# Performance work log

Measured on AMD Instinct MI355X. Metric: run time of the kernel, lower is better.

Reference implementation:

```python
import jax, jax.numpy as jnp
from jax import lax
import numpy as np

T, B, I, H = 512, 256, 13, 512


def setup_inputs() -> dict:
    key = jax.random.key(0)
    ks = jax.random.split(key, 8)
    s_ih = 1.0 / np.sqrt(H)
    # PyTorch LSTM params: gates stacked in order (i, f, g, o)
    x = jax.random.normal(ks[0], (T, B, I), dtype=jnp.float32)
    W_ih = jax.random.uniform(ks[1], (4 * H, I), minval=-s_ih, maxval=s_ih, dtype=jnp.float32)
    W_hh = jax.random.uniform(ks[2], (4 * H, H), minval=-s_ih, maxval=s_ih, dtype=jnp.float32)
    b_ih = jax.random.uniform(ks[3], (4 * H,), minval=-s_ih, maxval=s_ih, dtype=jnp.float32)
    b_hh = jax.random.uniform(ks[4], (4 * H,), minval=-s_ih, maxval=s_ih, dtype=jnp.float32)
    W_out = jax.random.uniform(ks[5], (1, H), minval=-s_ih, maxval=s_ih, dtype=jnp.float32)
    b_out = jax.random.uniform(ks[6], (1,), minval=-s_ih, maxval=s_ih, dtype=jnp.float32)
    return {"x": x, "W_ih": W_ih, "W_hh": W_hh, "b_ih": b_ih, "b_hh": b_hh,
            "W_out": W_out, "b_out": b_out}


def reference(x, W_ih, W_hh, b_ih, b_hh, W_out, b_out):
    # Precompute input-to-hidden gate projections for all timesteps (one big GEMM).
    # xg: [T, B, 4H]
    xg = jnp.einsum('tbi,gi->tbg', x, W_ih) + b_ih + b_hh
    h0 = jnp.zeros((x.shape[1], W_hh.shape[1]), dtype=x.dtype)

    def step(carry, xg_t):
        h, c = carry
        g = xg_t + h @ W_hh.T                      # [B, 4H]
        i, f, gg, o = jnp.split(g, 4, axis=-1)     # PyTorch gate order i,f,g,o
        i = jax.nn.sigmoid(i)
        f = jax.nn.sigmoid(f)
        gg = jnp.tanh(gg)
        o = jax.nn.sigmoid(o)
        c = f * c + i * gg
        h = o * jnp.tanh(c)
        return (h, c), h

    _, hs = lax.scan(step, (h0, h0), xg)           # hs: [T, B, H]
    y = jax.nn.relu(hs) @ W_out.T + b_out          # [T, B, 1]
    return y
```

## Files before the change

kernel.cpp:

```cpp
#include <hip/hip_runtime.h>
#include <hip/hip_bf16.h>

#define TT 512
#define BB 256
#define II 13
#define HH 512
#define NBLK 256
#define NTH 256
#define NKT 17
#define NSL 34
#define PS2 (NSL * 512)
#define GST 18
#define XROW (BB * II)

typedef __attribute__((ext_vector_type(8))) short short8;
typedef __attribute__((ext_vector_type(4))) float floatx4;
typedef __attribute__((ext_vector_type(4))) int intx4;

__device__ inline float sigm(float v) { return 1.f / (1.f + __expf(-v)); }
__device__ inline float tanh_(float v) {
    float e = __expf(-2.f * fabsf(v));
    float t = (1.f - e) / (1.f + e);
    return v < 0.f ? -t : t;
}
__device__ inline void split_bits(float v, unsigned short* hi, unsigned short* lo) {
    __hip_bfloat16 h = __float2bfloat16(v);
    float r = v - __bfloat162float(h);
    __hip_bfloat16 l = __float2bfloat16(r);
    *hi = __builtin_bit_cast(unsigned short, h);
    *lo = __builtin_bit_cast(unsigned short, l);
}
__device__ inline unsigned short bf16_bits(float v) {
    return __builtin_bit_cast(unsigned short, __float2bfloat16(v));
}

__device__ inline unsigned poll_mall(const unsigned* p) {
    unsigned v;
    asm volatile("global_load_dword %0, %1, off sc0 sc1\n\ts_waitcnt vmcnt(0)"
                 : "=&v"(v) : "v"(p) : "memory");
    return v;
}
__device__ inline void arrive_mall(unsigned* p) {
    asm volatile("global_atomic_add %0, %1, off sc1" :: "v"(p), "v"(1u) : "memory");
}
__device__ inline intx4 load_b128_l2(const void* p) {
    intx4 v;
    asm volatile("global_load_dwordx4 %0, %1, off sc0" : "=v"(v) : "v"(p));
    return v;
}
__device__ inline void store_short_l2(void* p, unsigned short v) {
    unsigned vv = v;
    asm volatile("global_store_short %0, %1, off sc0" :: "v"(p), "v"(vv) : "memory");
}
__device__ inline void store_dword_l2(void* p, unsigned v) {
    asm volatile("global_store_dword %0, %1, off sc0" :: "v"(p), "v"(v) : "memory");
}
__device__ inline void store_f32_wt(float* p, float v) {
    asm volatile("global_store_dword %0, %1, off sc0 sc1" :: "v"(p), "v"(v) : "memory");
}

__device__ inline void barrier_xcd(unsigned* cnt, unsigned target) {
    __syncthreads();
    if (threadIdx.x == 0) {
        arrive_mall(cnt);
        int guard = 0;
        unsigned v;
        do { v = poll_mall(cnt); } while ((int)(v - target) < 0 && ++guard < (1 << 16));
    }
    __syncthreads();
}

__global__ void __launch_bounds__(NTH, 1)
lstm_persist(const float* __restrict__ X,   const float* __restrict__ Wih,
             const float* __restrict__ Whh, const float* __restrict__ bih,
             const float* __restrict__ bhh, const float* __restrict__ Wout,
             const float* __restrict__ bout, float* __restrict__ Y,
             unsigned short* __restrict__ hbuf, unsigned* __restrict__ bars)
{
    extern __shared__ char smem[];
    unsigned short* Wf = (unsigned short*)smem;
    float* gbuf = (float*)(Wf + 4 * 2 * NKT * 512);
    int* shint = (int*)(gbuf + 128 * GST);

    const int tid = threadIdx.x;

    if (tid == 0) {
        unsigned x = __builtin_amdgcn_s_getreg(20 | (3 << 11)) & 7u;
        unsigned r = __hip_atomic_fetch_add(bars + 256 + x * 16, 1u,
                        __ATOMIC_RELAXED, __HIP_MEMORY_SCOPE_AGENT);
        shint[0] = (int)x;
        shint[1] = (int)(r & 31u);
    }
    __syncthreads();
    const int bc = shint[0];
    const int hs = shint[1];
    unsigned* bcnt = bars + bc * 32;

#define REGION(buf) (((buf) * 8 + bc) * PS2)

    {
        unsigned* hw = (unsigned*)hbuf;
        store_dword_l2(hw + (REGION(0) >> 1) + hs * 256 + tid, 0u);
        store_dword_l2(hw + (REGION(1) >> 1) + hs * 256 + tid, 0u);
        if (hs == 0) {
            for (int e = tid; e < 2 * 1024; e += NTH) {
                int buf = e >> 10, off = e & 1023;
                int row = (off >> 4) & 31, col = off & 15;
                unsigned short vh = 0;
                if (off < 512) {
                    if (col == 13) vh = 0x3F80u;
                    else if (col < 13 && buf == 0)
                        vh = bf16_bits(X[(bc * 32 + row) * II + col]);
                }
                store_short_l2(hbuf + REGION(buf) + 32 * 512 + off, vh);
            }
        }
        const float b0 = bout[0];
        for (int i = tid; i < 16 * 32; i += NTH) {
            int tr = hs * 16 + (i >> 5), cb = bc * 32 + (i & 31);
            store_f32_wt(&Y[tr * BB + cb], b0);
        }
    }
    for (int n = 0; n < 64; ++n) {
        int gate = n >> 4, hl = n & 15;
        int gr = gate * HH + hs * 16 + hl;
        for (int k = tid; k < 544; k += NTH) {
            float v;
            if (k < HH)            v = Whh[gr * HH + k];
            else if (k < HH + II)  v = Wih[gr * II + (k - HH)];
            else if (k == HH + II) v = bih[gr] + bhh[gr];
            else                   v = 0.f;
            unsigned short hi, lo; split_bits(v, &hi, &lo);
            const int slot = (hl + 16 * ((k & 31) >> 3)) * 8 + (k & 7);
            Wf[((gate * 2 + 0) * NKT + (k >> 5)) * 512 + slot] = hi;
            Wf[((gate * 2 + 1) * NKT + (k >> 5)) * 512 + slot] = lo;
        }
    }
    const int e0 = 2 * tid;
    const bool stv = (e0 < 32 * II);
    const int bl0 = e0 / II, xc0 = e0 - bl0 * II;
    const int e1 = e0 + 1;
    const int bl1 = e1 / II, xc1 = e1 - bl1 * II;
    float xr0 = 0.f, xr1 = 0.f;
    if (hs == 1 && stv) {
        const float2 v = *(const float2*)(X + XROW + bc * (32 * II) + e0);
        xr0 = v.x; xr1 = v.y;
    }

    barrier_xcd(bcnt, 32u);

    const int lane = tid & 63, wid = tid >> 6;
    const int mt = wid & 1;
    const int gp = wid >> 1;
    const int r15  = lane & 15;
    const int kgo  = (lane >> 4) * 8;
    const int slb  = kgo >> 4;
    const int lanehoff = (mt * 16 + r15) * 16 + (kgo & 8);
    const int lane8 = lane * 8;
    const unsigned short* F0 = Wf + ((4 * gp + 0) * NKT) * 512 + lane8;
    const unsigned short* F1 = Wf + ((4 * gp + 1) * NKT) * 512 + lane8;
    const unsigned short* F2 = Wf + ((4 * gp + 2) * NKT) * 512 + lane8;
    const unsigned short* F3 = Wf + ((4 * gp + 3) * NKT) * 512 + lane8;
    float c0 = 0.f, c1 = 0.f;
    const int ebl2 = tid >> 3;
    const int ej   = (tid & 7) * 2;
    const float2 wout2 = *(const float2*)&Wout[hs * 16 + ej];

    float ypend = 0.f;
    int   ycur  = bc * 32 + ebl2;

    for (int t = 0; t < TT; ++t) {
        const int cur = t & 1, nxt = cur ^ 1;
        const unsigned short* Ac = hbuf + REGION(cur) + lanehoff;

        intx4 ah[NKT];
#pragma unroll
        for (int kt = 0; kt < NKT; ++kt)
            ah[kt] = load_b128_l2(Ac + (kt * 2 + slb) * 512);
        __builtin_amdgcn_sched_barrier(0);
        if ((tid & 7) == 0)
            atomicAdd(&Y[ycur], ypend);
        __builtin_amdgcn_sched_barrier(0);

        short8 w0[4], w1[4], w2[4], w3[4];
#pragma unroll
        for (int j = 0; j < 4; ++j) {
            w0[j] = *(const short8*)(F0 + j * 512);
            w1[j] = *(const short8*)(F1 + j * 512);
            w2[j] = *(const short8*)(F2 + j * 512);
            w3[j] = *(const short8*)(F3 + j * 512);
        }
        floatx4 aA0 = {0,0,0,0}, aB0 = {0,0,0,0};
        floatx4 aA1 = {0,0,0,0}, aB1 = {0,0,0,0};

        asm volatile("s_waitcnt vmcnt(10)" ::: "memory");
        __builtin_amdgcn_sched_barrier(0);
#pragma unroll
        for (int kt = 0; kt < 8; ++kt) {
            short8 bh0 = w0[kt & 3], bv0 = w1[kt & 3];
            short8 bh1 = w2[kt & 3], bv1 = w3[kt & 3];
            if (kt + 4 < NKT) {
                w0[kt & 3] = *(const short8*)(F0 + (kt + 4) * 512);
                w1[kt & 3] = *(const short8*)(F1 + (kt + 4) * 512);
                w2[kt & 3] = *(const short8*)(F2 + (kt + 4) * 512);
                w3[kt & 3] = *(const short8*)(F3 + (kt + 4) * 512);
            }
            short8 chi = __builtin_bit_cast(short8, ah[kt]);
            aA0 = __builtin_amdgcn_mfma_f32_16x16x32_bf16(chi, bh0, aA0, 0, 0, 0);
            aA1 = __builtin_amdgcn_mfma_f32_16x16x32_bf16(chi, bh1, aA1, 0, 0, 0);
            aB0 = __builtin_amdgcn_mfma_f32_16x16x32_bf16(chi, bv0, aB0, 0, 0, 0);
            aB1 = __builtin_amdgcn_mfma_f32_16x16x32_bf16(chi, bv1, aB1, 0, 0, 0);
        }
        asm volatile("s_waitcnt vmcnt(1)" ::: "memory");
        __builtin_amdgcn_sched_barrier(0);
#pragma unroll
        for (int kt = 8; kt < NKT; ++kt) {
            short8 bh0 = w0[kt & 3], bv0 = w1[kt & 3];
            short8 bh1 = w2[kt & 3], bv1 = w3[kt & 3];
            if (kt + 4 < NKT) {
                w0[kt & 3] = *(const short8*)(F0 + (kt + 4) * 512);
                w1[kt & 3] = *(const short8*)(F1 + (kt + 4) * 512);
                w2[kt & 3] = *(const short8*)(F2 + (kt + 4) * 512);
                w3[kt & 3] = *(const short8*)(F3 + (kt + 4) * 512);
            }
            short8 chi = __builtin_bit_cast(short8, ah[kt]);
            aA0 = __builtin_amdgcn_mfma_f32_16x16x32_bf16(chi, bh0, aA0, 0, 0, 0);
            aA1 = __builtin_amdgcn_mfma_f32_16x16x32_bf16(chi, bh1, aA1, 0, 0, 0);
            aB0 = __builtin_amdgcn_mfma_f32_16x16x32_bf16(chi, bv0, aB0, 0, 0, 0);
            aB1 = __builtin_amdgcn_mfma_f32_16x16x32_bf16(chi, bv1, aB1, 0, 0, 0);
        }
        floatx4 acc0 = aA0 + aB0;
        floatx4 acc1 = aA1 + aB1;

        {
            const int b0r = mt * 16 + (lane >> 4) * 4;
            const int g0 = gp * 2;
#pragma unroll
            for (int r = 0; r < 4; ++r) {
                gbuf[((g0    ) * 32 + b0r + r) * GST + r15] = acc0[r];
                gbuf[((g0 + 1) * 32 + b0r + r) * GST + r15] = acc1[r];
            }
        }
        __syncthreads();
        {
            const float2 gi = *(const float2*)&gbuf[(0 * 32 + ebl2) * GST + ej];
            const float2 gf = *(const float2*)&gbuf[(1 * 32 + ebl2) * GST + ej];
            const float2 gg = *(const float2*)&gbuf[(2 * 32 + ebl2) * GST + ej];
            const float2 go = *(const float2*)&gbuf[(3 * 32 + ebl2) * GST + ej];

            c0 = sigm(gf.x) * c0 + sigm(gi.x) * tanh_(gg.x);
            float ha = sigm(go.x) * tanh_(c0);
            c1 = sigm(gf.y) * c1 + sigm(gi.y) * tanh_(gg.y);
            float hb = sigm(go.y) * tanh_(c1);

            unsigned* hw = (unsigned*)hbuf;
            store_dword_l2(hw + (REGION(nxt) >> 1) + hs * 256 + ebl2 * 8 + (tid & 7),
                           (unsigned)bf16_bits(ha) | ((unsigned)bf16_bits(hb) << 16));

            float p = fmaxf(ha, 0.f) * wout2.x + fmaxf(hb, 0.f) * wout2.y;
#pragma unroll
            for (int s = 4; s >= 1; s >>= 1)
                p += __shfl_xor(p, s);
            ypend = p;
            ycur  = t * BB + bc * 32 + ebl2;
        }
        if (t + 1 < TT && hs == ((t + 1) & 31) && stv) {
            store_short_l2(hbuf + REGION(nxt) + 32 * 512 + bl0 * 16 + xc0,
                           bf16_bits(xr0));
            store_short_l2(hbuf + REGION(nxt) + 32 * 512 + bl1 * 16 + xc1,
                           bf16_bits(xr1));
        }
        if (t + 2 < TT && hs == ((t + 2) & 31) && stv) {
            const float2 v = *(const float2*)(X + (t + 2) * XROW + bc * (32 * II) + e0);
            xr0 = v.x; xr1 = v.y;
        }
        if (t + 1 < TT)
            barrier_xcd(bcnt, 32u * (unsigned)(t + 2));
    }
    if ((tid & 7) == 0)
        atomicAdd(&Y[ycur], ypend);
}

extern "C" void kernel_launch(void* const* d_in, const int* in_sizes, int n_in,
                              void* d_out, int out_size, void* d_ws, size_t ws_size,
                              hipStream_t stream) {
    (void)in_sizes; (void)n_in; (void)out_size; (void)ws_size;
    const float* X    = (const float*)d_in[0];
    const float* Wih  = (const float*)d_in[1];
    const float* Whh  = (const float*)d_in[2];
    const float* bih  = (const float*)d_in[3];
    const float* bhh  = (const float*)d_in[4];
    const float* Wout = (const float*)d_in[5];
    const float* bout = (const float*)d_in[6];
    float* Y = (float*)d_out;

    unsigned* bars = (unsigned*)d_ws;
    unsigned short* hbuf = (unsigned short*)((char*)d_ws + 2048);

    hipMemsetAsync(d_ws, 0, 2048, stream);

    const size_t lds = (size_t)(4 * 2 * NKT * 512 * 2) + 128 * GST * 4 + 16;
    hipFuncSetAttribute((const void*)lstm_persist,
                        hipFuncAttributeMaxDynamicSharedMemorySize, (int)lds);

    hipLaunchKernelGGL(lstm_persist, dim3(NBLK), dim3(NTH), lds, stream,
                       X, Wih, Whh, bih, bhh, Wout, bout, Y, hbuf, bars);
}
```

Baseline: 1.487 ms.

## Double block size to 512 threads, one gate per wave pair

Doubles threads per block from 256 to 512 so each pair of waves computes one gate instead of two, halving the MFMA chain and weight loads per wave on the serial per-timestep critical path. The elementwise LSTM update now runs one hidden unit per thread, packing bf16 pairs with a lane shuffle, and the output reduction widens to 16 lanes. The cost is more waves per CU and register pressure. It may hit occupancy or launch limits when all 256 persistent blocks must stay co-resident for the cross-block barrier.

```diff
diff --git a/kernel.cpp b/kernel.cpp
--- a/kernel.cpp
+++ b/kernel.cpp
@@ -6,7 +6,7 @@
 #define II 13
 #define HH 512
 #define NBLK 256
-#define NTH 256
+#define NTH 512
 #define NKT 17
 #define NSL 34
 #define PS2 (NSL * 512)
@@ -100,8 +100,10 @@
 
     {
         unsigned* hw = (unsigned*)hbuf;
-        store_dword_l2(hw + (REGION(0) >> 1) + hs * 256 + tid, 0u);
-        store_dword_l2(hw + (REGION(1) >> 1) + hs * 256 + tid, 0u);
+        if (tid < 256) {
+            store_dword_l2(hw + (REGION(0) >> 1) + hs * 256 + tid, 0u);
+            store_dword_l2(hw + (REGION(1) >> 1) + hs * 256 + tid, 0u);
+        }
         if (hs == 0) {
             for (int e = tid; e < 2 * 1024; e += NTH) {
                 int buf = e >> 10, off = e & 1023;
@@ -116,8 +118,8 @@
             }
         }
         const float b0 = bout[0];
-        for (int i = tid; i < 16 * 32; i += NTH) {
-            int tr = hs * 16 + (i >> 5), cb = bc * 32 + (i & 31);
+        {
+            int tr = hs * 16 + (tid >> 5), cb = bc * 32 + (tid & 31);
             store_f32_wt(&Y[tr * BB + cb], b0);
         }
     }
@@ -151,23 +153,21 @@
 
     const int lane = tid & 63, wid = tid >> 6;
     const int mt = wid & 1;
-    const int gp = wid >> 1;
+    const int g  = wid >> 1;
     const int r15  = lane & 15;
     const int kgo  = (lane >> 4) * 8;
     const int slb  = kgo >> 4;
     const int lanehoff = (mt * 16 + r15) * 16 + (kgo & 8);
     const int lane8 = lane * 8;
-    const unsigned short* F0 = Wf + ((4 * gp + 0) * NKT) * 512 + lane8;
-    const unsigned short* F1 = Wf + ((4 * gp + 1) * NKT) * 512 + lane8;
-    const unsigned short* F2 = Wf + ((4 * gp + 2) * NKT) * 512 + lane8;
-    const unsigned short* F3 = Wf + ((4 * gp + 3) * NKT) * 512 + lane8;
-    float c0 = 0.f, c1 = 0.f;
-    const int ebl2 = tid >> 3;
-    const int ej   = (tid & 7) * 2;
-    const float2 wout2 = *(const float2*)&Wout[hs * 16 + ej];
+    const unsigned short* FH = Wf + ((g * 2 + 0) * NKT) * 512 + lane8;
+    const unsigned short* FL = Wf + ((g * 2 + 1) * NKT) * 512 + lane8;
+    float cc = 0.f;
+    const int erow = tid >> 4;
+    const int ecol = tid & 15;
+    const float woutv = Wout[hs * 16 + ecol];
 
     float ypend = 0.f;
-    int   ycur  = bc * 32 + ebl2;
+    int   ycur  = bc * 32 + erow;
 
     for (int t = 0; t < TT; ++t) {
         const int cur = t & 1, nxt = cur ^ 1;
@@ -178,91 +178,76 @@
         for (int kt = 0; kt < NKT; ++kt)
             ah[kt] = load_b128_l2(Ac + (kt * 2 + slb) * 512);
         __builtin_amdgcn_sched_barrier(0);
-        if ((tid & 7) == 0)
+        if (ecol == 0)
             atomicAdd(&Y[ycur], ypend);
         __builtin_amdgcn_sched_barrier(0);
 
-        short8 w0[4], w1[4], w2[4], w3[4];
+        short8 wh[4], wl[4];
 #pragma unroll
         for (int j = 0; j < 4; ++j) {
-            w0[j] = *(const short8*)(F0 + j * 512);
-            w1[j] = *(const short8*)(F1 + j * 512);
-            w2[j] = *(const short8*)(F2 + j * 512);
-            w3[j] = *(const short8*)(F3 + j * 512);
-        }
-        floatx4 aA0 = {0,0,0,0}, aB0 = {0,0,0,0};
-        floatx4 aA1 = {0,0,0,0}, aB1 = {0,0,0,0};
+            wh[j] = *(const short8*)(FH + j * 512);
+            wl[j] = *(const short8*)(FL + j * 512);
+        }
+        floatx4 aA = {0,0,0,0}, aB = {0,0,0,0};
 
         asm volatile("s_waitcnt vmcnt(10)" ::: "memory");
         __builtin_amdgcn_sched_barrier(0);
 #pragma unroll
         for (int kt = 0; kt < 8; ++kt) {
-            short8 bh0 = w0[kt & 3], bv0 = w1[kt & 3];
-            short8 bh1 = w2[kt & 3], bv1 = w3[kt & 3];
+            short8 bh = wh[kt & 3], bv = wl[kt & 3];
             if (kt + 4 < NKT) {
-                w0[kt & 3] = *(const short8*)(F0 + (kt + 4) * 512);
-                w1[kt & 3] = *(const short8*)(F1 + (kt + 4) * 512);
-                w2[kt & 3] = *(const short8*)(F2 + (kt + 4) * 512);
-                w3[kt & 3] = *(const short8*)(F3 + (kt + 4) * 512);
+                wh[kt & 3] = *(const short8*)(FH + (kt + 4) * 512);
+                wl[kt & 3] = *(const short8*)(FL + (kt + 4) * 512);
             }
             short8 chi = __builtin_bit_cast(short8, ah[kt]);
-            aA0 = __builtin_amdgcn_mfma_f32_16x16x32_bf16(chi, bh0, aA0, 0, 0, 0);
-            aA1 = __builtin_amdgcn_mfma_f32_16x16x32_bf16(chi, bh1, aA1, 0, 0, 0);
-            aB0 = __builtin_amdgcn_mfma_f32_16x16x32_bf16(chi, bv0, aB0, 0, 0, 0);
-            aB1 = __builtin_amdgcn_mfma_f32_16x16x32_bf16(chi, bv1, aB1, 0, 0, 0);
+            aA = __builtin_amdgcn_mfma_f32_16x16x32_bf16(chi, bh, aA, 0, 0, 0);
+            aB = __builtin_amdgcn_mfma_f32_16x16x32_bf16(chi, bv, aB, 0, 0, 0);
         }
         asm volatile("s_waitcnt vmcnt(1)" ::: "memory");
         __builtin_amdgcn_sched_barrier(0);
 #pragma unroll
         for (int kt = 8; kt < NKT; ++kt) {
-            short8 bh0 = w0[kt & 3], bv0 = w1[kt & 3];
-            short8 bh1 = w2[kt & 3], bv1 = w3[kt & 3];
+            short8 bh = wh[kt & 3], bv = wl[kt & 3];
             if (kt + 4 < NKT) {
-                w0[kt & 3] = *(const short8*)(F0 + (kt + 4) * 512);
-                w1[kt & 3] = *(const short8*)(F1 + (kt + 4) * 512);
-                w2[kt & 3] = *(const short8*)(F2 + (kt + 4) * 512);
-                w3[kt & 3] = *(const short8*)(F3 + (kt + 4) * 512);
+                wh[kt & 3] = *(const short8*)(FH + (kt + 4) * 512);
+                wl[kt & 3] = *(const short8*)(FL + (kt + 4) * 512);
             }
             short8 chi = __builtin_bit_cast(short8, ah[kt]);
-            aA0 = __builtin_amdgcn_mfma_f32_16x16x32_bf16(chi, bh0, aA0, 0, 0, 0);
-            aA1 = __builtin_amdgcn_mfma_f32_16x16x32_bf16(chi, bh1, aA1, 0, 0, 0);
-            aB0 = __builtin_amdgcn_mfma_f32_16x16x32_bf16(chi, bv0, aB0, 0, 0, 0);
-            aB1 = __builtin_amdgcn_mfma_f32_16x16x32_bf16(chi, bv1, aB1, 0, 0, 0);
-        }
-        floatx4 acc0 = aA0 + aB0;
-        floatx4 acc1 = aA1 + aB1;
+            aA = __builtin_amdgcn_mfma_f32_16x16x32_bf16(chi, bh, aA, 0, 0, 0);
+            aB = __builtin_amdgcn_mfma_f32_16x16x32_bf16(chi, bv, aB, 0, 0, 0);
+        }
+        floatx4 acc = aA + aB;
 
         {
             const int b0r = mt * 16 + (lane >> 4) * 4;
-            const int g0 = gp * 2;
-#pragma unroll
-            for (int r = 0; r < 4; ++r) {
-                gbuf[((g0    ) * 32 + b0r + r) * GST + r15] = acc0[r];
-                gbuf[((g0 + 1) * 32 + b0r + r) * GST + r15] = acc1[r];
-            }
+#pragma unroll
+            for (int r = 0; r < 4; ++r)
+                gbuf[(g * 32 + b0r + r) * GST + r15] = acc[r];
         }
         __syncthreads();
         {
-            const float2 gi = *(const float2*)&gbuf[(0 * 32 + ebl2) * GST + ej];
-            const float2 gf = *(const float2*)&gbuf[(1 * 32 + ebl2) * GST + ej];
-            const float2 gg = *(const float2*)&gbuf[(2 * 32 + ebl2) * GST + ej];
-            const float2 go = *(const float2*)&gbuf[(3 * 32 + ebl2) * GST + ej];
-
-            c0 = sigm(gf.x) * c0 + sigm(gi.x) * tanh_(gg.x);
-            float ha = sigm(go.x) * tanh_(c0);
-            c1 = sigm(gf.y) * c1 + sigm(gi.y) * tanh_(gg.y);
-            float hb = sigm(go.y) * tanh_(c1);
-
-            unsigned* hw = (unsigned*)hbuf;
-            store_dword_l2(hw + (REGION(nxt) >> 1) + hs * 256 + ebl2 * 8 + (tid & 7),
-                           (unsigned)bf16_bits(ha) | ((unsigned)bf16_bits(hb) << 16));
-
-            float p = fmaxf(ha, 0.f) * wout2.x + fmaxf(hb, 0.f) * wout2.y;
-#pragma unroll
-            for (int s = 4; s >= 1; s >>= 1)
+            float gi = gbuf[(0 * 32 + erow) * GST + ecol];
+            float gf = gbuf[(1 * 32 + erow) * GST + ecol];
+            float gg = gbuf[(2 * 32 + erow) * GST + ecol];
+            float go = gbuf[(3 * 32 + erow) * GST + ecol];
+
+            cc = sigm(gf) * cc + sigm(gi) * tanh_(gg);
+            float h = sigm(go) * tanh_(cc);
+
+            unsigned short hb = bf16_bits(h);
+            unsigned short hn = (unsigned short)__shfl_xor((int)hb, 1);
+            if ((ecol & 1) == 0) {
+                unsigned* hw = (unsigned*)hbuf;
+                store_dword_l2(hw + (REGION(nxt) >> 1) + hs * 256 + erow * 8 + (ecol >> 1),
+                               (unsigned)hb | ((unsigned)hn << 16));
+            }
+
+            float p = fmaxf(h, 0.f) * woutv;
+#pragma unroll
+            for (int s = 8; s >= 1; s >>= 1)
                 p += __shfl_xor(p, s);
             ypend = p;
-            ycur  = t * BB + bc * 32 + ebl2;
+            ycur  = t * BB + bc * 32 + erow;
         }
         if (t + 1 < TT && hs == ((t + 1) & 31) && stv) {
             store_short_l2(hbuf + REGION(nxt) + 32 * 512 + bl0 * 16 + xc0,
@@ -277,7 +262,7 @@
         if (t + 1 < TT)
             barrier_xcd(bcnt, 32u * (unsigned)(t + 2));
     }
-    if ((tid & 7) == 0)
+    if (ecol == 0)
         atomicAdd(&Y[ycur], ypend);
 }
 
```

Measured after the change: 3.420 ms. 130% more time.
